# Performance work log

Measured on AMD Instinct MI355X. Metric: run time of the kernel, lower is better.

Reference implementation:

```python
import jax, jax.numpy as jnp
import numpy as np

N, E, H, C, NG = 50000, 800000, 4, 64, 32
HC = H * C  # 256


def setup_inputs() -> dict:
    key = jax.random.key(0)
    ks = jax.random.split(key, 32)
    f32 = jnp.float32
    def rn(k, shape, s=0.1):
        return jax.random.normal(k, shape, dtype=f32) * s
    inp = {}
    inp['x'] = jax.random.normal(ks[0], (N, 4), dtype=f32)
    inp['edge_index'] = jax.random.randint(ks[1], (2, E), 0, N, dtype=jnp.int32)
    inp['edge_attr'] = jax.random.normal(ks[2], (E, 1), dtype=f32)
    inp['batch'] = jnp.sort(jax.random.randint(ks[3], (N,), 0, NG, dtype=jnp.int32))
    # encoder
    inp['enc_w'] = rn(ks[4], (4, 64)); inp['enc_b'] = rn(ks[5], (64,))
    # GATv2 layer 1: in 64 -> H*C (lin_l source, lin_r target, lin_edge, att, bias)
    inp['g1_wl'] = rn(ks[6], (64, HC)); inp['g1_bl'] = rn(ks[7], (HC,))
    inp['g1_wr'] = rn(ks[8], (64, HC)); inp['g1_br'] = rn(ks[9], (HC,))
    inp['g1_we'] = rn(ks[10], (1, HC))
    inp['g1_att'] = rn(ks[11], (H, C))
    inp['g1_bias'] = rn(ks[12], (HC,))
    # GATv2 layer 2: in 256 -> H*C
    inp['g2_wl'] = rn(ks[13], (HC, HC)); inp['g2_bl'] = rn(ks[14], (HC,))
    inp['g2_wr'] = rn(ks[15], (HC, HC)); inp['g2_br'] = rn(ks[16], (HC,))
    inp['g2_we'] = rn(ks[17], (1, HC))
    inp['g2_att'] = rn(ks[18], (H, C))
    inp['g2_bias'] = rn(ks[19], (HC,))
    # post MLP: 256 -> 128 (LayerNorm, ReLU) -> 64 (ReLU)
    inp['p1_w'] = rn(ks[20], (HC, 128)); inp['p1_b'] = rn(ks[21], (128,))
    inp['ln_g'] = jnp.ones((128,), dtype=f32); inp['ln_b'] = jnp.zeros((128,), dtype=f32)
    inp['p2_w'] = rn(ks[22], (128, 64)); inp['p2_b'] = rn(ks[23], (64,))
    return inp


def _gatv2_layer(x, src, dst, eattr, wl, bl, wr, br, we, att, bias):
    # PyG GATv2Conv: alpha_e = att . leaky_relu(lin_l(x_src) + lin_r(x_dst) + lin_edge(e))
    n = x.shape[0]
    xl = (x @ wl + bl).reshape(n, H, C)   # source-side messages
    xr = (x @ wr + br).reshape(n, H, C)   # target-side
    e = (eattr @ we).reshape(-1, H, C)
    m = jax.nn.leaky_relu(xl[src] + xr[dst] + e, 0.2)        # [E',H,C]
    alpha = jnp.einsum('ehc,hc->eh', m, att)                  # [E',H]
    amax = jax.lax.stop_gradient(jax.ops.segment_max(alpha, dst, num_segments=n))
    ex = jnp.exp(alpha - amax[dst])
    den = jax.ops.segment_sum(ex, dst, num_segments=n)
    a = ex / den[dst]                                          # softmax per dst node
    out = jax.ops.segment_sum(a[:, :, None] * xl[src], dst, num_segments=n)
    return out.reshape(n, HC) + bias


def reference(x, edge_index, edge_attr, batch, enc_w, enc_b,
              g1_wl, g1_bl, g1_wr, g1_br, g1_we, g1_att, g1_bias,
              g2_wl, g2_bl, g2_wr, g2_br, g2_we, g2_att, g2_bias,
              p1_w, p1_b, ln_g, ln_b, p2_w, p2_b):
    n = x.shape[0]
    src0, dst0 = edge_index[0], edge_index[1]
    # PyG default add_self_loops=True with fill_value='mean' for edge_attr
    deg = jnp.maximum(jax.ops.segment_sum(jnp.ones_like(edge_attr[:, 0]), dst0, num_segments=n), 1.0)
    loop_attr = jax.ops.segment_sum(edge_attr, dst0, num_segments=n) / deg[:, None]
    idx = jnp.arange(n, dtype=src0.dtype)
    src = jnp.concatenate([src0, idx]); dst = jnp.concatenate([dst0, idx])
    eattr = jnp.concatenate([edge_attr, loop_attr], axis=0)
    h = jax.nn.relu(x @ enc_w + enc_b)
    h = jax.nn.relu(_gatv2_layer(h, src, dst, eattr, g1_wl, g1_bl, g1_wr, g1_br, g1_we, g1_att, g1_bias))
    h = jax.nn.relu(_gatv2_layer(h, src, dst, eattr, g2_wl, g2_bl, g2_wr, g2_br, g2_we, g2_att, g2_bias))
    # global mean pool over graphs
    cnt = jnp.maximum(jax.ops.segment_sum(jnp.ones((n,), h.dtype), batch, num_segments=NG), 1.0)
    g = jax.ops.segment_sum(h, batch, num_segments=NG) / cnt[:, None]
    # post MLP (dropout is identity in eval)
    z = g @ p1_w + p1_b
    mu = jnp.mean(z, axis=-1, keepdims=True)
    var = jnp.mean((z - mu) ** 2, axis=-1, keepdims=True)
    z = (z - mu) / jnp.sqrt(var + 1e-5) * ln_g + ln_b
    z = jax.nn.relu(z)
    z = jax.nn.relu(z @ p2_w + p2_b)
    return z
```

## Files before the change

kernel.cpp:

```cpp
#include <hip/hip_runtime.h>

#define CDIV(a,b) (((a)+(b)-1)/(b))

typedef __bf16 bf16_t;
typedef unsigned char u8;
typedef bf16_t bf16x8 __attribute__((ext_vector_type(8)));
typedef float floatx4 __attribute__((ext_vector_type(4)));
typedef float floatx2 __attribute__((ext_vector_type(2)));

__device__ __forceinline__ int sigma2(int p) {
    int tile = p >> 7, hh = (p >> 6) & 1, m = (p >> 2) & 15, c = p & 3;
    return tile * 128 + (hh * 4 + c) * 16 + m;
}

__device__ __forceinline__ unsigned pack4_fp8(float a, float b, float c, float d) {
    int v = __builtin_amdgcn_cvt_pk_fp8_f32(a, b, 0, false);
    v = __builtin_amdgcn_cvt_pk_fp8_f32(c, d, v, true);
    return (unsigned)v;
}

template<bool HI>
__device__ __forceinline__ floatx2 cvtf8(unsigned v) {
    return __builtin_amdgcn_cvt_pk_f32_fp8(v, HI);
}

template<int CTRL>
__device__ __forceinline__ float dpp_add(float x) {
    int v = __builtin_amdgcn_update_dpp(0, __float_as_int(x), CTRL, 0xf, 0xf, true);
    return x + __int_as_float(v);
}

__global__ void k_deg(const int* __restrict__ ei, int* __restrict__ deg, int E) {
    int e = blockIdx.x * 256 + threadIdx.x;
    if (e >= E) return;
    atomicAdd(&deg[ei[E + e]], 1);
}

__global__ void k_scanA(const int* __restrict__ deg, int* __restrict__ part,
                        int* __restrict__ blockcnt, int n, int nb) {
    __shared__ int sh[256];
    __shared__ int h[64];
    int t = threadIdx.x;
    if (t < 64) h[t] = 0;
    int i = blockIdx.x * 256 + t;
    int v = (i < n) ? deg[i] : 0;
    __syncthreads();
    if (i < n) {
        int d = v > 63 ? 63 : v;
        atomicAdd(&h[63 - d], 1);
    }
    sh[t] = v;
    __syncthreads();
    for (int d = 128; d > 0; d >>= 1) { if (t < d) sh[t] += sh[t + d]; __syncthreads(); }
    if (t == 0) part[blockIdx.x] = sh[0];
    if (t < 64) blockcnt[t * nb + blockIdx.x] = h[t];
}
__global__ void k_bucketA(const int* __restrict__ bc, int* __restrict__ bpart, int total) {
    __shared__ int sh[256];
    int t = threadIdx.x;
    int i = blockIdx.x * 256 + t;
    sh[t] = (i < total) ? bc[i] : 0;
    __syncthreads();
    for (int d = 128; d > 0; d >>= 1) { if (t < d) sh[t] += sh[t + d]; __syncthreads(); }
    if (t == 0) bpart[blockIdx.x] = sh[0];
}
__global__ void k_scanB2(int* __restrict__ part, int nb,
                         int* __restrict__ bpart, int nbb) {
    __shared__ int sh[256];
    int t = threadIdx.x;
    int v = (t < nb) ? part[t] : 0;
    sh[t] = v;
    __syncthreads();
    for (int d = 1; d < 256; d <<= 1) {
        int u = (t >= d) ? sh[t - d] : 0;
        __syncthreads();
        sh[t] += u;
        __syncthreads();
    }
    if (t < nb) part[t] = sh[t] - v;
    __syncthreads();
    int v2 = (t < nbb) ? bpart[t] : 0;
    sh[t] = v2;
    __syncthreads();
    for (int d = 1; d < 256; d <<= 1) {
        int u = (t >= d) ? sh[t - d] : 0;
        __syncthreads();
        sh[t] += u;
        __syncthreads();
    }
    if (t < nbb) bpart[t] = sh[t] - v2;
}
__global__ void k_scanC(const int* __restrict__ deg, const int* __restrict__ part,
                        int* __restrict__ off, int n) {
    __shared__ int sh[256];
    int t = threadIdx.x;
    int i = blockIdx.x * 256 + t;
    int v = (i < n) ? deg[i] : 0;
    sh[t] = v;
    __syncthreads();
    for (int d = 1; d < 256; d <<= 1) {
        int u = (t >= d) ? sh[t - d] : 0;
        __syncthreads();
        sh[t] += u;
        __syncthreads();
    }
    int excl = part[blockIdx.x] + sh[t] - v;
    if (i < n) off[i] = excl;
    if (i == n - 1) off[n] = excl + v;
}
__global__ void k_bucketC(const int* __restrict__ bc, const int* __restrict__ bpart,
                          int* __restrict__ bo, int total) {
    __shared__ int sh[256];
    int t = threadIdx.x;
    int i = blockIdx.x * 256 + t;
    int v = (i < total) ? bc[i] : 0;
    sh[t] = v;
    __syncthreads();
    for (int d = 1; d < 256; d <<= 1) {
        int u = (t >= d) ? sh[t - d] : 0;
        __syncthreads();
        sh[t] += u;
        __syncthreads();
    }
    if (i < total) bo[i] = bpart[blockIdx.x] + sh[t] - v;
}
__global__ void k_scatter2(const int* __restrict__ deg, const int* __restrict__ bo,
                           int* __restrict__ perm, int n, int nb) {
    __shared__ int h[64];
    int t = threadIdx.x;
    if (t < 64) h[t] = 0;
    __syncthreads();
    int i = blockIdx.x * 256 + t;
    int b = 0, r = 0;
    if (i < n) {
        int d = deg[i]; if (d > 63) d = 63;
        b = 63 - d;
        r = atomicAdd(&h[b], 1);
    }
    __syncthreads();
    if (i < n) perm[bo[b * nb + blockIdx.x] + r] = i;
}

__global__ void k_fill(const int* __restrict__ ei, const float* __restrict__ ea,
                       const int* __restrict__ off, int* __restrict__ cursor,
                       int2* __restrict__ csr, int E) {
    int e = blockIdx.x * 256 + threadIdx.x;
    if (e >= E) return;
    int s = ei[e], d = ei[E + e];
    int pos = off[d] + atomicAdd(&cursor[d], 1);
    csr[pos] = make_int2(s, __float_as_int(ea[e]));
}

__global__ void k_wcast2(const float* __restrict__ Wl, const float* __restrict__ Wr,
                         const float* __restrict__ bl, const float* __restrict__ br,
                         bf16_t* __restrict__ Wt, float* __restrict__ bias2,
                         int K, int kshift, int permK,
                         const float* __restrict__ we, const float* __restrict__ att,
                         const float* __restrict__ cb,
                         float* __restrict__ wep, float* __restrict__ attp,
                         float* __restrict__ cbp) {
    int idx = blockIdx.x * 256 + threadIdx.x;
    if (idx < 512) bias2[idx] = (idx < 256) ? bl[idx] : br[idx - 256];
    if (idx < 256) {
        int sg = sigma2(idx);
        wep[idx] = we[sg]; attp[idx] = att[sg]; cbp[idx] = cb[sg];
    }
    if (idx >= 512 * K) return;
    int nn = idx >> kshift, k = idx & (K - 1);
    int ks = permK ? sigma2(k) : k;
    float v = (nn < 256) ? Wl[ks * 256 + nn] : Wr[ks * 256 + (nn - 256)];
    Wt[idx] = (bf16_t)v;
}

__global__ __launch_bounds__(256) void k_gemm1_fused(
        const float* __restrict__ x, const float* __restrict__ encw,
        const float* __restrict__ encb, const bf16_t* __restrict__ Wt,
        const float* __restrict__ bias2, u8* __restrict__ XL,
        u8* __restrict__ XR, int nrows) {
    __shared__ bf16_t As[128 * 32];
    __shared__ bf16_t Bs[128 * 32];
    int tid = threadIdx.x;
    int w = tid >> 6, lane = tid & 63;
    int quad = lane >> 4, m = lane & 15;
    int row0 = blockIdx.x * 128;
    int ct0 = blockIdx.y * 2;
    bf16x8 afr[2][2];
    floatx4 acc[2][8];

    for (int ctile = ct0; ctile < ct0 + 2; ++ctile) {
        int n0 = ctile * 128;
#pragma unroll
        for (int rt = 0; rt < 2; ++rt)
#pragma unroll
            for (int ct = 0; ct < 8; ++ct)
                acc[rt][ct] = (floatx4){0.f, 0.f, 0.f, 0.f};
        for (int k0c = 0; k0c < 2; ++k0c) {
            __syncthreads();
            if (ctile == ct0) {
#pragma unroll
                for (int i = 0; i < 2; ++i) {
                    int c = tid + i * 256;
                    int r = c >> 2, kc = c & 3;
                    int sw = (kc + (r >> 1)) & 3;
                    int gr = row0 + r; if (gr >= nrows) gr = nrows - 1;
                    float4 xv = ((const float4*)x)[gr];
                    bf16x8 v;
#pragma unroll
                    for (int kk = 0; kk < 8; ++kk) {
                        int k = k0c * 32 + kc * 8 + kk;
                        float s = encb[k];
                        s = fmaf(xv.x, encw[k], s);
                        s = fmaf(xv.y, encw[64 + k], s);
                        s = fmaf(xv.z, encw[128 + k], s);
                        s = fmaf(xv.w, encw[192 + k], s);
                        v[kk] = (bf16_t)fmaxf(s, 0.0f);
                    }
                    *(bf16x8*)&As[r * 32 + sw * 8] = v;
                }
            }
#pragma unroll
            for (int i = 0; i < 2; ++i) {
                int c = tid + i * 256;
                int r = c >> 2, kc = c & 3;
                int sw = (kc + (r >> 1)) & 3;
                bf16x8 v = *(const bf16x8*)&Wt[(size_t)(n0 + r) * 64 + k0c * 32 + kc * 8];
                *(bf16x8*)&Bs[r * 32 + sw * 8] = v;
            }
            __syncthreads();
            if (ctile == ct0) {
#pragma unroll
                for (int rt = 0; rt < 2; ++rt) {
                    int ar = w * 32 + rt * 16 + m;
                    afr[k0c][rt] = *(bf16x8*)&As[ar * 32 + (((quad + (ar >> 1)) & 3) * 8)];
                }
            }
            bf16x8 bfr[8];
#pragma unroll
            for (int ct = 0; ct < 8; ++ct) {
                int br = ct * 16 + m;
                bfr[ct] = *(bf16x8*)&Bs[br * 32 + (((quad + (br >> 1)) & 3) * 8)];
            }
#pragma unroll
            for (int ct = 0; ct < 8; ++ct) {
                acc[0][ct] = __builtin_amdgcn_mfma_f32_16x16x32_bf16(afr[k0c][0], bfr[ct], acc[0][ct], 0, 0, 0);
                acc[1][ct] = __builtin_amdgcn_mfma_f32_16x16x32_bf16(afr[k0c][1], bfr[ct], acc[1][ct], 0, 0, 0);
            }
        }
        int tile = ctile & 1;
        u8* dst = (ctile < 2) ? XL : XR;
        float bv[8];
#pragma unroll
        for (int ct = 0; ct < 8; ++ct) bv[ct] = bias2[n0 + ct * 16 + m];
#pragma unroll
        for (int rt = 0; rt < 2; ++rt) {
#pragma unroll
            for (int i = 0; i < 4; ++i) {
                int row = row0 + w * 32 + rt * 16 + quad * 4 + i;
                if (row < nrows) {
                    unsigned w0 = pack4_fp8(acc[rt][0][i] + bv[0], acc[rt][1][i] + bv[1],
                                            acc[rt][2][i] + bv[2], acc[rt][3][i] + bv[3]);
                    unsigned w1 = pack4_fp8(acc[rt][4][i] + bv[4], acc[rt][5][i] + bv[5],
                                            acc[rt][6][i] + bv[6], acc[rt][7][i] + bv[7]);
                    *(unsigned*)&dst[(size_t)row * 256 + tile * 128 + m * 4] = w0;
                    *(unsigned*)&dst[(size_t)row * 256 + tile * 128 + 64 + m * 4] = w1;
                }
            }
        }
    }
}

__global__ __launch_bounds__(256) void k_gemm2(
        const bf16_t* __restrict__ Hb, const bf16_t* __restrict__ Wt,
        const float* __restrict__ bias2, u8* __restrict__ XL,
        u8* __restrict__ XR, int nrows) {
    const int K = 256;
    __shared__ bf16_t As[128 * 32];
    __shared__ bf16_t Bs[128 * 32];
    int tid = threadIdx.x;
    int w = tid >> 6, lane = tid & 63;
    int quad = lane >> 4, m = lane & 15;
    int row0 = blockIdx.x * 128;
    int ct0 = blockIdx.y * 2;
    bf16x8 afr[8][2];
    floatx4 acc[2][8];

    for (int ctile = ct0; ctile < ct0 + 2; ++ctile) {
        int n0 = ctile * 128;
#pragma unroll
        for (int rt = 0; rt < 2; ++rt)
#pragma unroll
            for (int ct = 0; ct < 8; ++ct)
                acc[rt][ct] = (floatx4){0.f, 0.f, 0.f, 0.f};
        for (int k0c = 0; k0c < 8; ++k0c) {
            __syncthreads();
            if (ctile == ct0) {
#pragma unroll
                for (int i = 0; i < 2; ++i) {
                    int c = tid + i * 256;
                    int r = c >> 2, kc = c & 3;
                    int sw = (kc + (r >> 1)) & 3;
                    int gr = row0 + r; if (gr >= nrows) gr = nrows - 1;
                    bf16x8 v = *(const bf16x8*)&Hb[(size_t)gr * K + k0c * 32 + kc * 8];
                    *(bf16x8*)&As[r * 32 + sw * 8] = v;
                }
            }
#pragma unroll
            for (int i = 0; i < 2; ++i) {
                int c = tid + i * 256;
                int r = c >> 2, kc = c & 3;
                int sw = (kc + (r >> 1)) & 3;
                bf16x8 v = *(const bf16x8*)&Wt[(size_t)(n0 + r) * K + k0c * 32 + kc * 8];
                *(bf16x8*)&Bs[r * 32 + sw * 8] = v;
            }
            __syncthreads();
            if (ctile == ct0) {
#pragma unroll
                for (int rt = 0; rt < 2; ++rt) {
                    int ar = w * 32 + rt * 16 + m;
                    afr[k0c][rt] = *(bf16x8*)&As[ar * 32 + (((quad + (ar >> 1)) & 3) * 8)];
                }
            }
            bf16x8 bfr[8];
#pragma unroll
            for (int ct = 0; ct < 8; ++ct) {
                int br = ct * 16 + m;
                bfr[ct] = *(bf16x8*)&Bs[br * 32 + (((quad + (br >> 1)) & 3) * 8)];
            }
#pragma unroll
            for (int ct = 0; ct < 8; ++ct) {
                acc[0][ct] = __builtin_amdgcn_mfma_f32_16x16x32_bf16(afr[k0c][0], bfr[ct], acc[0][ct], 0, 0, 0);
                acc[1][ct] = __builtin_amdgcn_mfma_f32_16x16x32_bf16(afr[k0c][1], bfr[ct], acc[1][ct], 0, 0, 0);
            }
        }
        int tile = ctile & 1;
        u8* dst = (ctile < 2) ? XL : XR;
        float bv[8];
#pragma unroll
        for (int ct = 0; ct < 8; ++ct) bv[ct] = bias2[n0 + ct * 16 + m];
#pragma unroll
        for (int rt = 0; rt < 2; ++rt) {
#pragma unroll
            for (int i = 0; i < 4; ++i) {
                int row = row0 + w * 32 + rt * 16 + quad * 4 + i;
                if (row < nrows) {
                    unsigned w0 = pack4_fp8(acc[rt][0][i] + bv[0], acc[rt][1][i] + bv[1],
                                            acc[rt][2][i] + bv[2], acc[rt][3][i] + bv[3]);
                    unsigned w1 = pack4_fp8(acc[rt][4][i] + bv[4], acc[rt][5][i] + bv[5],
                                            acc[rt][6][i] + bv[6], acc[rt][7][i] + bv[7]);
                    *(unsigned*)&dst[(size_t)row * 256 + tile * 128 + m * 4] = w0;
                    *(unsigned*)&dst[(size_t)row * 256 + tile * 128 + 64 + m * 4] = w1;
                }
            }
        }
    }
}

__global__ void k_conv(
                       const u8* __restrict__ XL, const u8* __restrict__ XR,
                       const float* __restrict__ wep, const float* __restrict__ attp,
                       const int2* __restrict__ csr,
                       const int* __restrict__ off, const float* __restrict__ cbp,
                       const int* __restrict__ perm,
                       bf16_t* __restrict__ outb, int n) {
    int wid = (blockIdx.x * 256 + threadIdx.x) >> 6;
    int lane = threadIdx.x & 63;
    if (wid >= n) return;
    int node = perm[wid];
    int l = lane & 31, half = lane >> 5;
    int loff = l * 8;
    uint2 ur = *(const uint2*)(XR + (size_t)node * 256 + loff);
    uint2 us = *(const uint2*)(XL + (size_t)node * 256 + loff);
    floatx2 xr01 = cvtf8<false>(ur.x);
    floatx2 xr23 = cvtf8<true>(ur.x);
    floatx2 xr45 = cvtf8<false>(ur.y);
    floatx2 xr67 = cvtf8<true>(ur.y);
    float4 wa = ((const float4*)wep)[2 * l], wb = ((const float4*)wep)[2 * l + 1];
    float4 aa = ((const float4*)attp)[2 * l], ab = ((const float4*)attp)[2 * l + 1];
    floatx2 wv01 = {wa.x, wa.y}, wv23 = {wa.z, wa.w};
    floatx2 wv45 = {wb.x, wb.y}, wv67 = {wb.z, wb.w};
    const float LOG2E = 1.44269504f;
    floatx2 av01 = {aa.x * LOG2E, aa.y * LOG2E}, av23 = {aa.z * LOG2E, aa.w * LOG2E};
    floatx2 av45 = {ab.x * LOG2E, ab.y * LOG2E}, av67 = {ab.z * LOG2E, ab.w * LOG2E};
    int p0 = off[node], p1 = off[node + 1];
    float s = 0.f, sea = 0.f;
    floatx2 a01 = {0.f, 0.f}, a23 = {0.f, 0.f}, a45 = {0.f, 0.f}, a67 = {0.f, 0.f};

    for (int base = p0; base < p1; base += 64) {
        int rem = p1 - base;
        int cnt = (rem < 64) ? rem : 64;
        int gp = base + lane; if (gp > p1 - 1) gp = p1 - 1;
        int2 ed = csr[gp];

        float ev = (lane < cnt) ? __int_as_float(ed.y) : 0.f;
        ev += __shfl_xor(ev, 1);  ev += __shfl_xor(ev, 2);
        ev += __shfl_xor(ev, 4);  ev += __shfl_xor(ev, 8);
        ev += __shfl_xor(ev, 16); ev += __shfl_xor(ev, 32);
        sea += ev;

        auto fetch = [&](int j, uint2& u, float& e) {
            int sl = j + half; if (sl >= cnt) sl = cnt - 1;
            int sx = __shfl(ed.x, sl);
            e = __int_as_float(__shfl(ed.y, sl));
            u = *(const uint2*)(XL + (unsigned)(sx * 256 + loff));
        };

        uint2 u0, u1, u2; float e0, e1, e2;
        fetch(0, u0, e0);
        fetch(2, u1, e1);
        fetch(4, u2, e2);

#pragma unroll 3
        for (int j = 0; j < cnt; j += 2) {
            uint2 un; float en;
            fetch(j + 6, un, en);
            floatx2 x01 = cvtf8<false>(u0.x);
            floatx2 x23 = cvtf8<true>(u0.x);
            floatx2 x45 = cvtf8<false>(u0.y);
            floatx2 x67 = cvtf8<true>(u0.y);
            floatx2 t01 = x01 + xr01 + e0 * wv01;
            floatx2 t23 = x23 + xr23 + e0 * wv23;
            floatx2 t45 = x45 + xr45 + e0 * wv45;
            floatx2 t67 = x67 + xr67 + e0 * wv67;
            t01 = __builtin_elementwise_max(t01, 0.2f * t01);
            t23 = __builtin_elementwise_max(t23, 0.2f * t23);
            t45 = __builtin_elementwise_max(t45, 0.2f * t45);
            t67 = __builtin_elementwise_max(t67, 0.2f * t67);
            floatx2 d = t01 * av01 + t23 * av23 + t45 * av45 + t67 * av67;
            float al = d.x + d.y;
            al = dpp_add<0xB1>(al);
            al = dpp_add<0x4E>(al);
            al = dpp_add<0x141>(al);
            float wg = (j + half < cnt) ? exp2f(al) : 0.0f;
            s += wg;
            a01 += wg * x01; a23 += wg * x23; a45 += wg * x45; a67 += wg * x67;
            u0 = u1; e0 = e1; u1 = u2; e1 = e2; u2 = un; e2 = en;
        }
    }

    s += __shfl_xor(s, 32);
    a01.x += __shfl_xor(a01.x, 32); a01.y += __shfl_xor(a01.y, 32);
    a23.x += __shfl_xor(a23.x, 32); a23.y += __shfl_xor(a23.y, 32);
    a45.x += __shfl_xor(a45.x, 32); a45.y += __shfl_xor(a45.y, 32);
    a67.x += __shfl_xor(a67.x, 32); a67.y += __shfl_xor(a67.y, 32);

    {
        float dg = (float)(p1 - p0);
        float la = sea / fmaxf(dg, 1.0f);
        floatx2 xs01 = cvtf8<false>(us.x);
        floatx2 xs23 = cvtf8<true>(us.x);
        floatx2 xs45 = cvtf8<false>(us.y);
        floatx2 xs67 = cvtf8<true>(us.y);
        floatx2 t01 = xs01 + xr01 + la * wv01;
        floatx2 t23 = xs23 + xr23 + la * wv23;
        floatx2 t45 = xs45 + xr45 + la * wv45;
        floatx2 t67 = xs67 + xr67 + la * wv67;
        t01 = __builtin_elementwise_max(t01, 0.2f * t01);
        t23 = __builtin_elementwise_max(t23, 0.2f * t23);
        t45 = __builtin_elementwise_max(t45, 0.2f * t45);
        t67 = __builtin_elementwise_max(t67, 0.2f * t67);
        floatx2 d = t01 * av01 + t23 * av23 + t45 * av45 + t67 * av67;
        float al = d.x + d.y;
        al = dpp_add<0xB1>(al);
        al = dpp_add<0x4E>(al);
        al = dpp_add<0x141>(al);
        float wg = exp2f(al);
        s += wg;
        a01 += wg * xs01; a23 += wg * xs23; a45 += wg * xs45; a67 += wg * xs67;
    }

    if (half == 0) {
        float inv = 1.0f / s;
        float4 ba = ((const float4*)cbp)[2 * l], bb = ((const float4*)cbp)[2 * l + 1];
        bf16x8 ob;
        ob[0] = (bf16_t)fmaxf(fmaf(a01.x, inv, ba.x), 0.f);
        ob[1] = (bf16_t)fmaxf(fmaf(a01.y, inv, ba.y), 0.f);
        ob[2] = (bf16_t)fmaxf(fmaf(a23.x, inv, ba.z), 0.f);
        ob[3] = (bf16_t)fmaxf(fmaf(a23.y, inv, ba.w), 0.f);
        ob[4] = (bf16_t)fmaxf(fmaf(a45.x, inv, bb.x), 0.f);
        ob[5] = (bf16_t)fmaxf(fmaf(a45.y, inv, bb.y), 0.f);
        ob[6] = (bf16_t)fmaxf(fmaf(a67.x, inv, bb.z), 0.f);
        ob[7] = (bf16_t)fmaxf(fmaf(a67.y, inv, bb.w), 0.f);
        *(bf16x8*)&outb[(size_t)node * 256 + l * 8] = ob;
    }
}

__global__ void k_pool(const bf16_t* __restrict__ h, const int* __restrict__ batch,
                       float* __restrict__ gsum, float* __restrict__ gcnt, int n) {
    int j = threadIdx.x;
    int start = blockIdx.x * 32;
    if (start >= n) return;
    int end = start + 32; if (end > n) end = n;
    int cur = batch[start];
    float acc = 0.0f, cnt = 0.0f;
    for (int i = start; i < end; ++i) {
        int g = batch[i];
        if (g != cur) {
            atomicAdd(&gsum[cur * 256 + j], acc);
            if (j == 0) atomicAdd(&gcnt[cur], cnt);
            acc = 0.0f; cnt = 0.0f; cur = g;
        }
        acc += (float)h[(size_t)i * 256 + j];
        cnt += 1.0f;
    }
    atomicAdd(&gsum[cur * 256 + j], acc);
    if (j == 0) atomicAdd(&gcnt[cur], cnt);
}

__global__ void k_mlp(const float* __restrict__ gsum, const float* __restrict__ gcnt,
                      const float* __restrict__ p1w, const float* __restrict__ p1b,
                      const float* __restrict__ lng, const float* __restrict__ lnb,
                      const float* __restrict__ p2w, const float* __restrict__ p2b,
                      float* __restrict__ out) {
    int g = blockIdx.x;
    int t = threadIdx.x;
    __shared__ float gv[256];
    __shared__ float z[128];
    __shared__ float red[128];
    float invc = 1.0f / fmaxf(gcnt[g], 1.0f);
    gv[sigma2(t)]       = gsum[g * 256 + t] * invc;
    gv[sigma2(t + 128)] = gsum[g * 256 + 128 + t] * invc;
    __syncthreads();
    float z1 = p1b[t];
    for (int k = 0; k < 256; ++k) z1 = fmaf(gv[k], p1w[k * 128 + t], z1);
    red[t] = z1;
    __syncthreads();
    for (int d = 64; d > 0; d >>= 1) { if (t < d) red[t] += red[t + d]; __syncthreads(); }
    float mu = red[0] * (1.0f / 128.0f);
    __syncthreads();
    float dz = z1 - mu;
    red[t] = dz * dz;
    __syncthreads();
    for (int d = 64; d > 0; d >>= 1) { if (t < d) red[t] += red[t + d]; __syncthreads(); }
    float var = red[0] * (1.0f / 128.0f);
    float zn = dz * rsqrtf(var + 1e-5f) * lng[t] + lnb[t];
    z[t] = fmaxf(zn, 0.0f);
    __syncthreads();
    if (t < 64) {
        float o = p2b[t];
        for (int k = 0; k < 128; ++k) o = fmaf(z[k], p2w[k * 64 + t], o);
        out[g * 64 + t] = fmaxf(o, 0.0f);
    }
}

extern "C" void kernel_launch(void* const* d_in, const int* in_sizes, int n_in,
                              void* d_out, int out_size, void* d_ws, size_t ws_size,
                              hipStream_t stream) {
    const float* x      = (const float*)d_in[0];
    const int*   ei     = (const int*)d_in[1];
    const float* ea     = (const float*)d_in[2];
    const int*   batch  = (const int*)d_in[3];
    const float* enc_w  = (const float*)d_in[4];
    const float* enc_b  = (const float*)d_in[5];
    const float* g1_wl  = (const float*)d_in[6];
    const float* g1_bl  = (const float*)d_in[7];
    const float* g1_wr  = (const float*)d_in[8];
    const float* g1_br  = (const float*)d_in[9];
    const float* g1_we  = (const float*)d_in[10];
    const float* g1_att = (const float*)d_in[11];
    const float* g1_bias= (const float*)d_in[12];
    const float* g2_wl  = (const float*)d_in[13];
    const float* g2_bl  = (const float*)d_in[14];
    const float* g2_wr  = (const float*)d_in[15];
    const float* g2_br  = (const float*)d_in[16];
    const float* g2_we  = (const float*)d_in[17];
    const float* g2_att = (const float*)d_in[18];
    const float* g2_bias= (const float*)d_in[19];
    const float* p1_w   = (const float*)d_in[20];
    const float* p1_b   = (const float*)d_in[21];
    const float* ln_g   = (const float*)d_in[22];
    const float* ln_b   = (const float*)d_in[23];
    const float* p2_w   = (const float*)d_in[24];
    const float* p2_b   = (const float*)d_in[25];
    float* out = (float*)d_out;

    const int N  = in_sizes[3];
    const int E  = in_sizes[1] / 2;
    const int EE = E + N;
    const int NB = CDIV(N, 256);
    const int NBT = 64 * NB;
    const int NBB = CDIV(NBT, 256);

    u8*     XL  = (u8*)d_ws;
    u8*     XR  = XL + (size_t)N * 256;
    bf16_t* Hb  = (bf16_t*)(XR + (size_t)N * 256);
    bf16_t* Wt  = Hb + (size_t)N * 256;
    int2*  csr  = (int2*)(Wt + 512 * 256);
    float* gsum  = (float*)(csr + EE);
    float* gcnt  = gsum + 32 * 256;
    int*   deg   = (int*)(gcnt + 32);
    int*   cursor= deg + N;
    float* bias2 = (float*)(cursor + N);
    float* wep   = bias2 + 512;
    float* attp  = wep + 256;
    float* cbp   = attp + 256;
    int*   part  = (int*)(cbp + 256);
    int*   off   = part + 256;
    int*   perm  = off + (N + 1);
    int*   blockcnt = perm + N;
    int*   blockoff = blockcnt + NBT;
    int*   bpart    = blockoff + NBT;

    (void)hipMemsetAsync(gsum, 0, (size_t)(2 * N + 32 * 256 + 32) * sizeof(float), stream);

    k_deg<<<CDIV(E, 256), 256, 0, stream>>>(ei, deg, E);
    k_scanA<<<NB, 256, 0, stream>>>(deg, part, blockcnt, N, NB);
    k_bucketA<<<NBB, 256, 0, stream>>>(blockcnt, bpart, NBT);
    k_scanB2<<<1, 256, 0, stream>>>(part, NB, bpart, NBB);
    k_scanC<<<NB, 256, 0, stream>>>(deg, part, off, N);
    k_bucketC<<<NBB, 256, 0, stream>>>(blockcnt, bpart, blockoff, NBT);
    k_scatter2<<<NB, 256, 0, stream>>>(deg, blockoff, perm, N, NB);
    k_fill<<<CDIV(E, 256), 256, 0, stream>>>(ei, ea, off, cursor, csr, E);

    dim3 ggrid(CDIV(N, 128), 2);

    k_wcast2<<<CDIV(512 * 64, 256), 256, 0, stream>>>(g1_wl, g1_wr, g1_bl, g1_br, Wt, bias2,
                                                      64, 6, 0, g1_we, g1_att, g1_bias,
                                                      wep, attp, cbp);
    k_gemm1_fused<<<ggrid, 256, 0, stream>>>(x, enc_w, enc_b, Wt, bias2, XL, XR, N);
    k_conv<<<CDIV(N, 4), 256, 0, stream>>>(XL, XR, wep, attp, csr, off, cbp, perm, Hb, N);

    k_wcast2<<<CDIV(512 * 256, 256), 256, 0, stream>>>(g2_wl, g2_wr, g2_bl, g2_br, Wt, bias2,
                                                       256, 8, 1, g2_we, g2_att, g2_bias,
                                                       wep, attp, cbp);
    k_gemm2<<<ggrid, 256, 0, stream>>>(Hb, Wt, bias2, XL, XR, N);
    k_conv<<<CDIV(N, 4), 256, 0, stream>>>(XL, XR, wep, attp, csr, off, cbp, perm, Hb, N);

    k_pool<<<CDIV(N, 32), 256, 0, stream>>>(Hb, batch, gsum, gcnt, N);
    k_mlp<<<32, 128, 0, stream>>>(gsum, gcnt, p1_w, p1_b, ln_g, ln_b, p2_w, p2_b, out);
}
```

Measured before the change: 433.9 us.

## Store self-loops as explicit CSR entries with precomputed mean edge attribute

Self-loops are now written into the CSR as a real last entry per node, with the mean incoming edge attribute precomputed through an atomic sum in the degree kernel. The conv kernel drops its per-chunk wavefront reduction of edge attributes and the separate epilogue that handled the self-loop. The self-loop then goes through the main loop like any other edge. This adds a float atomic per edge and one extra CSR entry per node, and it shifts the offsets by one per node.

```diff
diff --git a/kernel.cpp b/kernel.cpp
--- a/kernel.cpp
+++ b/kernel.cpp
@@ -30,10 +30,13 @@
     return x + __int_as_float(v);
 }
 
-__global__ void k_deg(const int* __restrict__ ei, int* __restrict__ deg, int E) {
+__global__ void k_deg(const int* __restrict__ ei, const float* __restrict__ ea,
+                      int* __restrict__ deg, float* __restrict__ easum, int E) {
     int e = blockIdx.x * 256 + threadIdx.x;
     if (e >= E) return;
-    atomicAdd(&deg[ei[E + e]], 1);
+    int d = ei[E + e];
+    atomicAdd(&deg[d], 1);
+    atomicAdd(&easum[d], ea[e]);
 }
 
 __global__ void k_scanA(const int* __restrict__ deg, int* __restrict__ part,
@@ -43,13 +46,13 @@
     int t = threadIdx.x;
     if (t < 64) h[t] = 0;
     int i = blockIdx.x * 256 + t;
-    int v = (i < n) ? deg[i] : 0;
+    int dv = (i < n) ? deg[i] : -1;
     __syncthreads();
     if (i < n) {
-        int d = v > 63 ? 63 : v;
+        int d = dv > 63 ? 63 : dv;
         atomicAdd(&h[63 - d], 1);
     }
-    sh[t] = v;
+    sh[t] = (i < n) ? dv + 1 : 0;
     __syncthreads();
     for (int d = 128; d > 0; d >>= 1) { if (t < d) sh[t] += sh[t + d]; __syncthreads(); }
     if (t == 0) part[blockIdx.x] = sh[0];
@@ -95,7 +98,7 @@
     __shared__ int sh[256];
     int t = threadIdx.x;
     int i = blockIdx.x * 256 + t;
-    int v = (i < n) ? deg[i] : 0;
+    int v = (i < n) ? deg[i] + 1 : 0;
     sh[t] = v;
     __syncthreads();
     for (int d = 1; d < 256; d <<= 1) {
@@ -125,20 +128,27 @@
     if (i < total) bo[i] = bpart[blockIdx.x] + sh[t] - v;
 }
 __global__ void k_scatter2(const int* __restrict__ deg, const int* __restrict__ bo,
+                           const float* __restrict__ easum, const int* __restrict__ off,
+                           int2* __restrict__ csr,
                            int* __restrict__ perm, int n, int nb) {
     __shared__ int h[64];
     int t = threadIdx.x;
     if (t < 64) h[t] = 0;
     __syncthreads();
     int i = blockIdx.x * 256 + t;
-    int b = 0, r = 0;
+    int b = 0, r = 0, dv = 0;
     if (i < n) {
-        int d = deg[i]; if (d > 63) d = 63;
+        dv = deg[i];
+        int d = dv > 63 ? 63 : dv;
         b = 63 - d;
         r = atomicAdd(&h[b], 1);
     }
     __syncthreads();
-    if (i < n) perm[bo[b * nb + blockIdx.x] + r] = i;
+    if (i < n) {
+        perm[bo[b * nb + blockIdx.x] + r] = i;
+        float la = easum[i] / fmaxf((float)dv, 1.0f);
+        csr[off[i + 1] - 1] = make_int2(i, __float_as_int(la));
+    }
 }
 
 __global__ void k_fill(const int* __restrict__ ei, const float* __restrict__ ea,
@@ -369,7 +379,6 @@
     int l = lane & 31, half = lane >> 5;
     int loff = l * 8;
     uint2 ur = *(const uint2*)(XR + (size_t)node * 256 + loff);
-    uint2 us = *(const uint2*)(XL + (size_t)node * 256 + loff);
     floatx2 xr01 = cvtf8<false>(ur.x);
     floatx2 xr23 = cvtf8<true>(ur.x);
     floatx2 xr45 = cvtf8<false>(ur.y);
@@ -382,7 +391,7 @@
     floatx2 av01 = {aa.x * LOG2E, aa.y * LOG2E}, av23 = {aa.z * LOG2E, aa.w * LOG2E};
     floatx2 av45 = {ab.x * LOG2E, ab.y * LOG2E}, av67 = {ab.z * LOG2E, ab.w * LOG2E};
     int p0 = off[node], p1 = off[node + 1];
-    float s = 0.f, sea = 0.f;
+    float s = 0.f;
     floatx2 a01 = {0.f, 0.f}, a23 = {0.f, 0.f}, a45 = {0.f, 0.f}, a67 = {0.f, 0.f};
 
     for (int base = p0; base < p1; base += 64) {
@@ -391,16 +400,10 @@
         int gp = base + lane; if (gp > p1 - 1) gp = p1 - 1;
         int2 ed = csr[gp];
 
-        float ev = (lane < cnt) ? __int_as_float(ed.y) : 0.f;
-        ev += __shfl_xor(ev, 1);  ev += __shfl_xor(ev, 2);
-        ev += __shfl_xor(ev, 4);  ev += __shfl_xor(ev, 8);
-        ev += __shfl_xor(ev, 16); ev += __shfl_xor(ev, 32);
-        sea += ev;
-
-        auto fetch = [&](int j, uint2& u, float& e) {
+        auto fetch = [&](int j, uint2& u, float& ev) {
             int sl = j + half; if (sl >= cnt) sl = cnt - 1;
             int sx = __shfl(ed.x, sl);
-            e = __int_as_float(__shfl(ed.y, sl));
+            ev = __int_as_float(__shfl(ed.y, sl));
             u = *(const uint2*)(XL + (unsigned)(sx * 256 + loff));
         };
 
@@ -442,32 +445,6 @@
     a23.x += __shfl_xor(a23.x, 32); a23.y += __shfl_xor(a23.y, 32);
     a45.x += __shfl_xor(a45.x, 32); a45.y += __shfl_xor(a45.y, 32);
     a67.x += __shfl_xor(a67.x, 32); a67.y += __shfl_xor(a67.y, 32);
-
-    {
-        float dg = (float)(p1 - p0);
-        float la = sea / fmaxf(dg, 1.0f);
-        floatx2 xs01 = cvtf8<false>(us.x);
-        floatx2 xs23 = cvtf8<true>(us.x);
-        floatx2 xs45 = cvtf8<false>(us.y);
-        floatx2 xs67 = cvtf8<true>(us.y);
-        floatx2 t01 = xs01 + xr01 + la * wv01;
-        floatx2 t23 = xs23 + xr23 + la * wv23;
-        floatx2 t45 = xs45 + xr45 + la * wv45;
-        floatx2 t67 = xs67 + xr67 + la * wv67;
-        t01 = __builtin_elementwise_max(t01, 0.2f * t01);
-        t23 = __builtin_elementwise_max(t23, 0.2f * t23);
-        t45 = __builtin_elementwise_max(t45, 0.2f * t45);
-        t67 = __builtin_elementwise_max(t67, 0.2f * t67);
-        floatx2 d = t01 * av01 + t23 * av23 + t45 * av45 + t67 * av67;
-        float al = d.x + d.y;
-        al = dpp_add<0xB1>(al);
-        al = dpp_add<0x4E>(al);
-        al = dpp_add<0x141>(al);
-        float wg = exp2f(al);
-        s += wg;
-        a01 += wg * xs01; a23 += wg * xs23; a45 += wg * xs45; a67 += wg * xs67;
-    }
-
     if (half == 0) {
         float inv = 1.0f / s;
         float4 ba = ((const float4*)cbp)[2 * l], bb = ((const float4*)cbp)[2 * l + 1];
@@ -589,7 +566,8 @@
     float* gcnt  = gsum + 32 * 256;
     int*   deg   = (int*)(gcnt + 32);
     int*   cursor= deg + N;
-    float* bias2 = (float*)(cursor + N);
+    float* easum = (float*)(cursor + N);
+    float* bias2 = easum + N;
     float* wep   = bias2 + 512;
     float* attp  = wep + 256;
     float* cbp   = attp + 256;
@@ -600,15 +578,15 @@
     int*   blockoff = blockcnt + NBT;
     int*   bpart    = blockoff + NBT;
 
-    (void)hipMemsetAsync(gsum, 0, (size_t)(2 * N + 32 * 256 + 32) * sizeof(float), stream);
-
-    k_deg<<<CDIV(E, 256), 256, 0, stream>>>(ei, deg, E);
+    (void)hipMemsetAsync(gsum, 0, (size_t)(3 * N + 32 * 256 + 32) * sizeof(float), stream);
+
+    k_deg<<<CDIV(E, 256), 256, 0, stream>>>(ei, ea, deg, easum, E);
     k_scanA<<<NB, 256, 0, stream>>>(deg, part, blockcnt, N, NB);
     k_bucketA<<<NBB, 256, 0, stream>>>(blockcnt, bpart, NBT);
     k_scanB2<<<1, 256, 0, stream>>>(part, NB, bpart, NBB);
     k_scanC<<<NB, 256, 0, stream>>>(deg, part, off, N);
     k_bucketC<<<NBB, 256, 0, stream>>>(blockcnt, bpart, blockoff, NBT);
-    k_scatter2<<<NB, 256, 0, stream>>>(deg, blockoff, perm, N, NB);
+    k_scatter2<<<NB, 256, 0, stream>>>(deg, blockoff, easum, off, csr, perm, N, NB);
     k_fill<<<CDIV(E, 256), 256, 0, stream>>>(ei, ea, off, cursor, csr, E);
 
     dim3 ggrid(CDIV(N, 128), 2);
```

Result: slower. 453.5 us (+4.5%).
